# Kernel optimization log

Hardware: AMD Instinct MI355X
Metric: run time of the kernel (lower is better)

## Reference

```python
import jax, jax.numpy as jnp
import numpy as np

N_GROUP, D, DFF = 8, 256, 1024
T = 131072  # total routed tokens


def setup_inputs() -> dict:
    key = jax.random.key(0)
    k_x, k_g, k_u, k_d = jax.random.split(key, 4)
    # kaiming_uniform_(a=sqrt(5)) over fan_in == second-to-last dim
    def kaiming(k, shape, fan_in):
        bound = 1.0 / np.sqrt(fan_in)
        return jax.random.uniform(k, shape, jnp.float32, -bound, bound)
    x = jax.random.normal(k_x, (T, D), jnp.float32)
    weight_gate = kaiming(k_g, (N_GROUP, D, DFF), D)
    weight_up = kaiming(k_u, (N_GROUP, D, DFF), D)
    weight_down = kaiming(k_d, (N_GROUP, DFF, D), DFF)
    # cumulative group end offsets; uniform groups of T // N_GROUP tokens
    offs = (jnp.arange(1, N_GROUP + 1, dtype=jnp.int32) * (T // N_GROUP))
    return {"x": x, "weight_gate": weight_gate, "weight_up": weight_up,
            "weight_down": weight_down, "offs": offs}


def reference(x, weight_gate, weight_up, weight_down, offs):
    # Grouped GLU: for tokens in group g, y = silu(x @ Wg_gate) * (x @ Wg_up) @ Wg_down.
    # offs encodes uniform group boundaries (offs[i] = (i+1)*T/G), so the grouped
    # GEMM is a batched matmul over the expert axis after a reshape.
    G = weight_gate.shape[0]
    t, d = x.shape
    xg = x.reshape(G, t // G, d)                                  # [G, Tg, d]
    z_gate = jnp.einsum('gtd,gdf->gtf', xg, weight_gate)          # [G, Tg, dff]
    z_up = jnp.einsum('gtd,gdf->gtf', xg, weight_up)
    h = jax.nn.silu(z_gate) * z_up
    y = jnp.einsum('gtf,gfd->gtd', h, weight_down)                # [G, Tg, d]
    return y.reshape(t, d)
```

## Files before the change

### kernel.cpp

```cpp
#include <hip/hip_runtime.h>

typedef __bf16 bf16x8 __attribute__((ext_vector_type(8)));
typedef float f32x16 __attribute__((ext_vector_type(16)));
typedef unsigned int u32x4 __attribute__((ext_vector_type(4)));

#define NGROUP 8
#define DMODEL 256
#define DFF    1024
#define TTOT   131072
#define TGRP   (TTOT / NGROUP)
#define MTILE  256
#define NCHUNK 32

__device__ __forceinline__ unsigned int f2bf(float f) {
    unsigned int x = __builtin_bit_cast(unsigned int, f);
    return (x + 0x7fffu + ((x >> 16) & 1u)) >> 16;
}
__device__ __forceinline__ unsigned int pack2(float lo, float hi) {
    return f2bf(lo) | (f2bf(hi) << 16);
}
__device__ __forceinline__ unsigned int cvtpk(float lo, float hi) {
    unsigned int r;
    asm("v_cvt_pk_bf16_f32 %0, %1, %2" : "=v"(r) : "v"(lo), "v"(hi));
    return r;
}

__device__ __forceinline__ void g2l(const void* g, void* l) {
    __builtin_amdgcn_global_load_lds(
        (const __attribute__((address_space(1))) unsigned int*)g,
        (__attribute__((address_space(3))) unsigned int*)l, 16, 0, 0);
}

__global__ void k_prep_w(const float* __restrict__ wg, const float* __restrict__ wu,
                         const float* __restrict__ wd, u32x4* __restrict__ out) {
    int t = blockIdx.x * 256 + threadIdx.x;
    int lane = t & 63;
    int q = lane >> 5, l31 = lane & 31;
    int fg = t >> 6;
    int fid = fg % 48;
    int gc  = fg / 48;
    int c = gc & 31, g = gc >> 5;
    u32x4 v;
    if (fid < 32) {
        const float* w = (fid < 16) ? wg : wu;
        int ks = fid & 15;
        const float* src = w + (size_t)(g * 256 + ks * 16 + q * 8) * 1024 + c * 32 + l31;
        v = u32x4{ pack2(src[0],        src[1024]),
                   pack2(src[2 * 1024], src[3 * 1024]),
                   pack2(src[4 * 1024], src[5 * 1024]),
                   pack2(src[6 * 1024], src[7 * 1024]) };
    } else {
        int idx = fid - 32;
        int ks2 = idx >> 3, nb = idx & 7;
        const float* src = wd + (size_t)(g * 1024 + c * 32 + ks2 * 16 + q * 4) * 256 + nb * 32 + l31;
        v = u32x4{ pack2(src[0 * 256],  src[1 * 256]),
                   pack2(src[2 * 256],  src[3 * 256]),
                   pack2(src[8 * 256],  src[9 * 256]),
                   pack2(src[10 * 256], src[11 * 256]) };
    }
    out[t] = v;
}

#define MFMA(A, B, C) __builtin_amdgcn_mfma_f32_32x32x16_bf16( \
        __builtin_bit_cast(bf16x8, A), __builtin_bit_cast(bf16x8, B), C, 0, 0, 0)

__global__ __launch_bounds__(512, 2)
void k_glu(const float* __restrict__ x,
           const u32x4* __restrict__ wcomb,
           float* __restrict__ y) {
    __shared__ u32x4 smem[9216];

    const int tid  = threadIdx.x;
    const int lane = tid & 63;
    const int w    = tid >> 6;
    const int q    = lane >> 5;
    const int l31  = lane & 31;

    const int g    = blockIdx.x & 7;
    const int m0   = g * TGRP + (blockIdx.x >> 3) * MTILE;
    const int tok  = m0 + w * 32 + l31;

    const u32x4* wcg = wcomb + (size_t)(g * 32) * 3072;

    #pragma unroll
    for (int i = 0; i < 6; ++i) {
        int off = i * 512 + w * 64;
        g2l(wcg + off + lane, smem + off);
    }
    #pragma unroll
    for (int i = 0; i < 6; ++i) {
        int off = i * 512 + w * 64;
        g2l(wcg + 3072 + off + lane, smem + 3072 + off);
    }
    u32x4 xf[16];
    {
        const float* xrow = x + (size_t)tok * DMODEL + q * 8;
        #pragma unroll
        for (int ks = 0; ks < 16; ++ks) {
            float4 a = *(const float4*)(xrow + ks * 16);
            float4 b = *(const float4*)(xrow + ks * 16 + 4);
            xf[ks] = u32x4{ cvtpk(a.x, a.y), cvtpk(a.z, a.w),
                            cvtpk(b.x, b.y), cvtpk(b.z, b.w) };
        }
    }

    f32x16 acc[8];
    #pragma unroll
    for (int nb = 0; nb < 8; ++nb)
        #pragma unroll
        for (int i = 0; i < 16; ++i) acc[nb][i] = 0.0f;

    asm volatile("s_waitcnt vmcnt(0)" ::: "memory");
    __builtin_amdgcn_s_barrier();
    asm volatile("" ::: "memory");

    u32x4 A0, A1;

    {
        const u32x4* sb = smem;
        f32x16 zg, zu;
        #pragma unroll
        for (int i = 0; i < 16; ++i) { zg[i] = 0.0f; zu[i] = 0.0f; }
        #pragma unroll
        for (int ks = 0; ks < 16; ++ks) {
            const u32x4 a1 = sb[ks * 64 + lane];
            const u32x4 a2 = sb[1024 + ks * 64 + lane];
            zg = MFMA(a1, xf[ks], zg);
            zu = MFMA(a2, xf[ks], zu);
        }
        float hv[16];
        #pragma unroll
        for (int i = 0; i < 16; ++i) {
            const float gv = zg[i];
            const float s  = __builtin_amdgcn_rcpf(1.0f + __expf(-gv));
            hv[i] = gv * s * zu[i];
        }
        A0 = u32x4{ cvtpk(hv[0], hv[1]),   cvtpk(hv[2], hv[3]),
                    cvtpk(hv[4], hv[5]),   cvtpk(hv[6], hv[7]) };
        A1 = u32x4{ cvtpk(hv[8], hv[9]),   cvtpk(hv[10], hv[11]),
                    cvtpk(hv[12], hv[13]), cvtpk(hv[14], hv[15]) };
    }

    int bc = 1, bp = 0, bn = 2;
    for (int c = 1; c < NCHUNK; ++c) {
        const u32x4* sbc = smem + bc * 3072;
        const u32x4* sbp = smem + bp * 3072;

        asm volatile("s_waitcnt vmcnt(0)" ::: "memory");
        __builtin_amdgcn_s_barrier();
        asm volatile("" ::: "memory");

        if (c + 1 < NCHUNK) {
            u32x4* db = smem + bn * 3072;
            const u32x4* gsrc = wcg + (size_t)(c + 1) * 3072;
            #pragma unroll
            for (int i = 0; i < 6; ++i) {
                int off = i * 512 + w * 64;
                g2l(gsrc + off + lane, db + off);
            }
        }

        f32x16 zg, zu;
        #pragma unroll
        for (int i = 0; i < 16; ++i) { zg[i] = 0.0f; zu[i] = 0.0f; }
        #pragma unroll
        for (int ks = 0; ks < 16; ++ks) {
            const u32x4 a1 = sbc[ks * 64 + lane];
            const u32x4 a2 = sbc[1024 + ks * 64 + lane];
            const u32x4 bd = sbp[2048 + ks * 64 + lane];
            zg = MFMA(a1, xf[ks], zg);
            zu = MFMA(a2, xf[ks], zu);
            if (ks < 8) acc[ks]     = MFMA(A0, bd, acc[ks]);
            else        acc[ks - 8] = MFMA(A1, bd, acc[ks - 8]);
        }

        float hv[16];
        #pragma unroll
        for (int i = 0; i < 16; ++i) {
            const float gv = zg[i];
            const float s  = __builtin_amdgcn_rcpf(1.0f + __expf(-gv));
            hv[i] = gv * s * zu[i];
        }
        A0 = u32x4{ cvtpk(hv[0], hv[1]),   cvtpk(hv[2], hv[3]),
                    cvtpk(hv[4], hv[5]),   cvtpk(hv[6], hv[7]) };
        A1 = u32x4{ cvtpk(hv[8], hv[9]),   cvtpk(hv[10], hv[11]),
                    cvtpk(hv[12], hv[13]), cvtpk(hv[14], hv[15]) };

        const int t = bp; bp = bc; bc = bn; bn = t;
    }

    {
        const u32x4* sbp = smem + bp * 3072;
        #pragma unroll
        for (int ks = 0; ks < 16; ++ks) {
            const u32x4 bd = sbp[2048 + ks * 64 + lane];
            if (ks < 8) acc[ks]     = MFMA(A0, bd, acc[ks]);
            else        acc[ks - 8] = MFMA(A1, bd, acc[ks - 8]);
        }
    }

    float* yp = y + (size_t)(m0 + w * 32) * DMODEL;
    #pragma unroll
    for (int nb = 0; nb < 8; ++nb) {
        const int col = nb * 32 + l31;
        #pragma unroll
        for (int r = 0; r < 16; ++r) {
            const int row = (r & 3) + (r >> 2) * 8 + q * 4;
            yp[(size_t)row * DMODEL + col] = acc[nb][r];
        }
    }
}

extern "C" void kernel_launch(void* const* d_in, const int* in_sizes, int n_in,
                              void* d_out, int out_size, void* d_ws, size_t ws_size,
                              hipStream_t stream) {
    const float* x  = (const float*)d_in[0];
    const float* wg = (const float*)d_in[1];
    const float* wu = (const float*)d_in[2];
    const float* wd = (const float*)d_in[3];
    float* y = (float*)d_out;

    u32x4* wcomb = (u32x4*)d_ws;

    k_prep_w<<<dim3(3072), dim3(256), 0, stream>>>(wg, wu, wd, wcomb);
    k_glu<<<dim3(512), dim3(512), 0, stream>>>(x, wcomb, y);
}
```

Measured before the change: 414.9 us.

## Give each wave two 32-token row tiles and prefetch weight chunks two ahead

Blocks shrink from 512 to 256 threads and each wave now processes 64 tokens as two 32-row tiles. Every weight fragment read from LDS therefore feeds two MFMAs, halving LDS traffic per FLOP. The cross-chunk software pipeline, which overlapped the down-projection of chunk c-1 with the gate/up of chunk c, is replaced by a triple buffer that prefetches two chunks ahead with partial vmcnt waits. s_setprio is added around the MFMA blocks. The cost is much higher register use: two x fragment sets and two accumulator sets per wave, with launch bounds set to one block. Occupancy also drops to 4 waves per block.

```diff
diff --git a/kernel.cpp b/kernel.cpp
--- a/kernel.cpp
+++ b/kernel.cpp
@@ -64,7 +64,7 @@
 #define MFMA(A, B, C) __builtin_amdgcn_mfma_f32_32x32x16_bf16( \
         __builtin_bit_cast(bf16x8, A), __builtin_bit_cast(bf16x8, B), C, 0, 0, 0)
 
-__global__ __launch_bounds__(512, 2)
+__global__ __launch_bounds__(256, 1)
 void k_glu(const float* __restrict__ x,
            const u32x4* __restrict__ wcomb,
            float* __restrict__ y) {
@@ -78,135 +78,151 @@
 
     const int g    = blockIdx.x & 7;
     const int m0   = g * TGRP + (blockIdx.x >> 3) * MTILE;
-    const int tok  = m0 + w * 32 + l31;
+    const int tok0 = m0 + w * 64 + l31;
+    const int tok1 = tok0 + 32;
 
     const u32x4* wcg = wcomb + (size_t)(g * 32) * 3072;
 
     #pragma unroll
-    for (int i = 0; i < 6; ++i) {
-        int off = i * 512 + w * 64;
+    for (int i = 0; i < 12; ++i) {
+        int off = i * 256 + w * 64;
         g2l(wcg + off + lane, smem + off);
     }
     #pragma unroll
-    for (int i = 0; i < 6; ++i) {
-        int off = i * 512 + w * 64;
+    for (int i = 0; i < 12; ++i) {
+        int off = i * 256 + w * 64;
         g2l(wcg + 3072 + off + lane, smem + 3072 + off);
     }
-    u32x4 xf[16];
+    u32x4 xf0[16], xf1[16];
     {
-        const float* xrow = x + (size_t)tok * DMODEL + q * 8;
+        const float* xr0 = x + (size_t)tok0 * DMODEL + q * 8;
+        const float* xr1 = x + (size_t)tok1 * DMODEL + q * 8;
         #pragma unroll
         for (int ks = 0; ks < 16; ++ks) {
-            float4 a = *(const float4*)(xrow + ks * 16);
-            float4 b = *(const float4*)(xrow + ks * 16 + 4);
-            xf[ks] = u32x4{ cvtpk(a.x, a.y), cvtpk(a.z, a.w),
-                            cvtpk(b.x, b.y), cvtpk(b.z, b.w) };
-        }
-    }
-
-    f32x16 acc[8];
+            float4 a = *(const float4*)(xr0 + ks * 16);
+            float4 b = *(const float4*)(xr0 + ks * 16 + 4);
+            xf0[ks] = u32x4{ cvtpk(a.x, a.y), cvtpk(a.z, a.w),
+                             cvtpk(b.x, b.y), cvtpk(b.z, b.w) };
+            float4 cfour = *(const float4*)(xr1 + ks * 16);
+            float4 d = *(const float4*)(xr1 + ks * 16 + 4);
+            xf1[ks] = u32x4{ cvtpk(cfour.x, cfour.y), cvtpk(cfour.z, cfour.w),
+                             cvtpk(d.x, d.y), cvtpk(d.z, d.w) };
+        }
+    }
+
+    f32x16 acc0[8], acc1[8];
     #pragma unroll
     for (int nb = 0; nb < 8; ++nb)
         #pragma unroll
-        for (int i = 0; i < 16; ++i) acc[nb][i] = 0.0f;
+        for (int i = 0; i < 16; ++i) { acc0[nb][i] = 0.0f; acc1[nb][i] = 0.0f; }
 
     asm volatile("s_waitcnt vmcnt(0)" ::: "memory");
     __builtin_amdgcn_s_barrier();
     asm volatile("" ::: "memory");
 
-    u32x4 A0, A1;
-
-    {
-        const u32x4* sb = smem;
-        f32x16 zg, zu;
-        #pragma unroll
-        for (int i = 0; i < 16; ++i) { zg[i] = 0.0f; zu[i] = 0.0f; }
-        #pragma unroll
-        for (int ks = 0; ks < 16; ++ks) {
-            const u32x4 a1 = sb[ks * 64 + lane];
-            const u32x4 a2 = sb[1024 + ks * 64 + lane];
-            zg = MFMA(a1, xf[ks], zg);
-            zu = MFMA(a2, xf[ks], zu);
-        }
-        float hv[16];
-        #pragma unroll
-        for (int i = 0; i < 16; ++i) {
-            const float gv = zg[i];
-            const float s  = __builtin_amdgcn_rcpf(1.0f + __expf(-gv));
-            hv[i] = gv * s * zu[i];
-        }
-        A0 = u32x4{ cvtpk(hv[0], hv[1]),   cvtpk(hv[2], hv[3]),
-                    cvtpk(hv[4], hv[5]),   cvtpk(hv[6], hv[7]) };
-        A1 = u32x4{ cvtpk(hv[8], hv[9]),   cvtpk(hv[10], hv[11]),
-                    cvtpk(hv[12], hv[13]), cvtpk(hv[14], hv[15]) };
-    }
-
-    int bc = 1, bp = 0, bn = 2;
-    for (int c = 1; c < NCHUNK; ++c) {
+    int bc = 0;
+    for (int c = 0; c < NCHUNK; ++c) {
         const u32x4* sbc = smem + bc * 3072;
-        const u32x4* sbp = smem + bp * 3072;
-
-        asm volatile("s_waitcnt vmcnt(0)" ::: "memory");
-        __builtin_amdgcn_s_barrier();
-        asm volatile("" ::: "memory");
-
-        if (c + 1 < NCHUNK) {
+
+        if (c > 0) {
+            if (c <= NCHUNK - 2) {
+                asm volatile("s_waitcnt vmcnt(12)" ::: "memory");
+            } else {
+                asm volatile("s_waitcnt vmcnt(0)" ::: "memory");
+            }
+            __builtin_amdgcn_s_barrier();
+            asm volatile("" ::: "memory");
+        }
+
+        if (c + 2 < NCHUNK) {
+            const int bn = (bc + 2 >= 3) ? bc - 1 : bc + 2;
             u32x4* db = smem + bn * 3072;
-            const u32x4* gsrc = wcg + (size_t)(c + 1) * 3072;
-            #pragma unroll
-            for (int i = 0; i < 6; ++i) {
-                int off = i * 512 + w * 64;
+            const u32x4* gsrc = wcg + (size_t)(c + 2) * 3072;
+            #pragma unroll
+            for (int i = 0; i < 12; ++i) {
+                int off = i * 256 + w * 64;
                 g2l(gsrc + off + lane, db + off);
             }
         }
 
-        f32x16 zg, zu;
-        #pragma unroll
-        for (int i = 0; i < 16; ++i) { zg[i] = 0.0f; zu[i] = 0.0f; }
+        f32x16 zg0, zu0, zg1, zu1;
+        #pragma unroll
+        for (int i = 0; i < 16; ++i) { zg0[i] = 0.0f; zu0[i] = 0.0f; zg1[i] = 0.0f; zu1[i] = 0.0f; }
+        __builtin_amdgcn_s_setprio(1);
         #pragma unroll
         for (int ks = 0; ks < 16; ++ks) {
             const u32x4 a1 = sbc[ks * 64 + lane];
             const u32x4 a2 = sbc[1024 + ks * 64 + lane];
-            const u32x4 bd = sbp[2048 + ks * 64 + lane];
-            zg = MFMA(a1, xf[ks], zg);
-            zu = MFMA(a2, xf[ks], zu);
-            if (ks < 8) acc[ks]     = MFMA(A0, bd, acc[ks]);
-            else        acc[ks - 8] = MFMA(A1, bd, acc[ks - 8]);
-        }
-
-        float hv[16];
-        #pragma unroll
-        for (int i = 0; i < 16; ++i) {
-            const float gv = zg[i];
-            const float s  = __builtin_amdgcn_rcpf(1.0f + __expf(-gv));
-            hv[i] = gv * s * zu[i];
-        }
-        A0 = u32x4{ cvtpk(hv[0], hv[1]),   cvtpk(hv[2], hv[3]),
-                    cvtpk(hv[4], hv[5]),   cvtpk(hv[6], hv[7]) };
-        A1 = u32x4{ cvtpk(hv[8], hv[9]),   cvtpk(hv[10], hv[11]),
-                    cvtpk(hv[12], hv[13]), cvtpk(hv[14], hv[15]) };
-
-        const int t = bp; bp = bc; bc = bn; bn = t;
+            zg0 = MFMA(a1, xf0[ks], zg0);
+            zg1 = MFMA(a1, xf1[ks], zg1);
+            zu0 = MFMA(a2, xf0[ks], zu0);
+            zu1 = MFMA(a2, xf1[ks], zu1);
+        }
+        __builtin_amdgcn_s_setprio(0);
+
+        u32x4 A00, A01, A10, A11;
+        {
+            float hv[16];
+            #pragma unroll
+            for (int i = 0; i < 16; ++i) {
+                const float gv = zg0[i];
+                const float s  = __builtin_amdgcn_rcpf(1.0f + __expf(-gv));
+                hv[i] = gv * s * zu0[i];
+            }
+            A00 = u32x4{ cvtpk(hv[0], hv[1]),   cvtpk(hv[2], hv[3]),
+                         cvtpk(hv[4], hv[5]),   cvtpk(hv[6], hv[7]) };
+            A01 = u32x4{ cvtpk(hv[8], hv[9]),   cvtpk(hv[10], hv[11]),
+                         cvtpk(hv[12], hv[13]), cvtpk(hv[14], hv[15]) };
+            #pragma unroll
+            for (int i = 0; i < 16; ++i) {
+                const float gv = zg1[i];
+                const float s  = __builtin_amdgcn_rcpf(1.0f + __expf(-gv));
+                hv[i] = gv * s * zu1[i];
+            }
+            A10 = u32x4{ cvtpk(hv[0], hv[1]),   cvtpk(hv[2], hv[3]),
+                         cvtpk(hv[4], hv[5]),   cvtpk(hv[6], hv[7]) };
+            A11 = u32x4{ cvtpk(hv[8], hv[9]),   cvtpk(hv[10], hv[11]),
+                         cvtpk(hv[12], hv[13]), cvtpk(hv[14], hv[15]) };
+        }
+
+        __builtin_amdgcn_s_setprio(1);
+        #pragma unroll
+        for (int fi = 0; fi < 8; ++fi) {
+            const u32x4 bd = sbc[2048 + fi * 64 + lane];
+            acc0[fi] = MFMA(A00, bd, acc0[fi]);
+            acc1[fi] = MFMA(A10, bd, acc1[fi]);
+        }
+        #pragma unroll
+        for (int fi = 0; fi < 8; ++fi) {
+            const u32x4 bd = sbc[2048 + (8 + fi) * 64 + lane];
+            acc0[fi] = MFMA(A01, bd, acc0[fi]);
+            acc1[fi] = MFMA(A11, bd, acc1[fi]);
+        }
+        __builtin_amdgcn_s_setprio(0);
+
+        bc = (bc == 2) ? 0 : bc + 1;
     }
 
     {
-        const u32x4* sbp = smem + bp * 3072;
-        #pragma unroll
-        for (int ks = 0; ks < 16; ++ks) {
-            const u32x4 bd = sbp[2048 + ks * 64 + lane];
-            if (ks < 8) acc[ks]     = MFMA(A0, bd, acc[ks]);
-            else        acc[ks - 8] = MFMA(A1, bd, acc[ks - 8]);
-        }
-    }
-
-    float* yp = y + (size_t)(m0 + w * 32) * DMODEL;
-    #pragma unroll
-    for (int nb = 0; nb < 8; ++nb) {
-        const int col = nb * 32 + l31;
-        #pragma unroll
-        for (int r = 0; r < 16; ++r) {
-            const int row = (r & 3) + (r >> 2) * 8 + q * 4;
-            yp[(size_t)row * DMODEL + col] = acc[nb][r];
+        float* yp = y + (size_t)(m0 + w * 64) * DMODEL;
+        #pragma unroll
+        for (int nb = 0; nb < 8; ++nb) {
+            const int col = nb * 32 + l31;
+            #pragma unroll
+            for (int r = 0; r < 16; ++r) {
+                const int row = (r & 3) + (r >> 2) * 8 + q * 4;
+                yp[(size_t)row * DMODEL + col] = acc0[nb][r];
+            }
+        }
+        float* yq = yp + 32 * DMODEL;
+        #pragma unroll
+        for (int nb = 0; nb < 8; ++nb) {
+            const int col = nb * 32 + l31;
+            #pragma unroll
+            for (int r = 0; r < 16; ++r) {
+                const int row = (r & 3) + (r >> 2) * 8 + q * 4;
+                yq[(size_t)row * DMODEL + col] = acc1[nb][r];
+            }
         }
     }
 }
@@ -223,5 +239,5 @@
     u32x4* wcomb = (u32x4*)d_ws;
 
     k_prep_w<<<dim3(3072), dim3(256), 0, stream>>>(wg, wu, wd, wcomb);
-    k_glu<<<dim3(512), dim3(512), 0, stream>>>(x, wcomb, y);
-}
+    k_glu<<<dim3(512), dim3(256), 0, stream>>>(x, wcomb, y);
+}
```

After: 546.0 us. 31.6% more time.

## Split fused GLU into two GEMM kernels with bf16 intermediate buffer

Applied to the files above, without the earlier changes.

Replaces the single fused GLU kernel with two kernels. The first computes gate/up projections and SiLU for 64 tokens per wave and writes h in MFMA-fragment layout to a workspace buffer. The second runs the down projection with a 2x4 wave tiling and a triple-buffered, two-chunk-ahead load pipeline. This targets the low MFMA reuse of the fused kernel, where each wave handled 32 tokens, at the cost of writing and re-reading a 256 MB bf16 intermediate. The old fused kernel remains as a fallback when the workspace is too small.

```diff
diff --git a/kernel.cpp b/kernel.cpp
--- a/kernel.cpp
+++ b/kernel.cpp
@@ -9,8 +9,8 @@
 #define DFF    1024
 #define TTOT   131072
 #define TGRP   (TTOT / NGROUP)
-#define MTILE  256
 #define NCHUNK 32
+
 
 __device__ __forceinline__ unsigned int f2bf(float f) {
     unsigned int x = __builtin_bit_cast(unsigned int, f);
@@ -30,6 +30,9 @@
         (const __attribute__((address_space(1))) unsigned int*)g,
         (__attribute__((address_space(3))) unsigned int*)l, 16, 0, 0);
 }
+
+#define MFMA(A, B, C) __builtin_amdgcn_mfma_f32_32x32x16_bf16( \
+        __builtin_bit_cast(bf16x8, A), __builtin_bit_cast(bf16x8, B), C, 0, 0, 0)
 
 __global__ void k_prep_w(const float* __restrict__ wg, const float* __restrict__ wu,
                          const float* __restrict__ wd, u32x4* __restrict__ out) {
@@ -61,14 +64,10 @@
     out[t] = v;
 }
 
-#define MFMA(A, B, C) __builtin_amdgcn_mfma_f32_32x32x16_bf16( \
-        __builtin_bit_cast(bf16x8, A), __builtin_bit_cast(bf16x8, B), C, 0, 0, 0)
-
 __global__ __launch_bounds__(512, 2)
-void k_glu(const float* __restrict__ x,
-           const u32x4* __restrict__ wcomb,
-           float* __restrict__ y) {
-    __shared__ u32x4 smem[9216];
+void k_gemm1(const float* __restrict__ x, const u32x4* __restrict__ wcomb,
+             u32x4* __restrict__ hout) {
+    __shared__ u32x4 smem[4096];
 
     const int tid  = threadIdx.x;
     const int lane = tid & 63;
@@ -77,21 +76,213 @@
     const int l31  = lane & 31;
 
     const int g    = blockIdx.x & 7;
-    const int m0   = g * TGRP + (blockIdx.x >> 3) * MTILE;
-    const int tok  = m0 + w * 32 + l31;
+    const int m0   = g * TGRP + (blockIdx.x >> 3) * 512;
+    const int tok0 = m0 + w * 64 + l31;
+    const int tok1 = tok0 + 32;
+    const size_t tb0 = (size_t)((m0 >> 5) + w * 2);
 
     const u32x4* wcg = wcomb + (size_t)(g * 32) * 3072;
 
     #pragma unroll
-    for (int i = 0; i < 6; ++i) {
+    for (int i = 0; i < 4; ++i) {
         int off = i * 512 + w * 64;
         g2l(wcg + off + lane, smem + off);
     }
-    #pragma unroll
-    for (int i = 0; i < 6; ++i) {
-        int off = i * 512 + w * 64;
-        g2l(wcg + 3072 + off + lane, smem + 3072 + off);
-    }
+
+    u32x4 xf0[16], xf1[16];
+    {
+        const float* xr0 = x + (size_t)tok0 * DMODEL + q * 8;
+        const float* xr1 = x + (size_t)tok1 * DMODEL + q * 8;
+        #pragma unroll
+        for (int ks = 0; ks < 16; ++ks) {
+            float4 a = *(const float4*)(xr0 + ks * 16);
+            float4 b = *(const float4*)(xr0 + ks * 16 + 4);
+            xf0[ks] = u32x4{ cvtpk(a.x, a.y), cvtpk(a.z, a.w),
+                             cvtpk(b.x, b.y), cvtpk(b.z, b.w) };
+            float4 e = *(const float4*)(xr1 + ks * 16);
+            float4 d = *(const float4*)(xr1 + ks * 16 + 4);
+            xf1[ks] = u32x4{ cvtpk(e.x, e.y), cvtpk(e.z, e.w),
+                             cvtpk(d.x, d.y), cvtpk(d.z, d.w) };
+        }
+    }
+
+    for (int c = 0; c < NCHUNK; ++c) {
+        const u32x4* sbc = smem + (c & 1) * 2048;
+
+        asm volatile("s_waitcnt vmcnt(0)" ::: "memory");
+        __builtin_amdgcn_s_barrier();
+        asm volatile("" ::: "memory");
+
+        if (c + 1 < NCHUNK) {
+            u32x4* db = smem + ((c + 1) & 1) * 2048;
+            const u32x4* gsrc = wcg + (size_t)(c + 1) * 3072;
+            #pragma unroll
+            for (int i = 0; i < 4; ++i) {
+                int off = i * 512 + w * 64;
+                g2l(gsrc + off + lane, db + off);
+            }
+        }
+
+        f32x16 zg0, zu0, zg1, zu1;
+        #pragma unroll
+        for (int i = 0; i < 16; ++i) { zg0[i] = 0.0f; zu0[i] = 0.0f; zg1[i] = 0.0f; zu1[i] = 0.0f; }
+        __builtin_amdgcn_s_setprio(1);
+        #pragma unroll
+        for (int ks = 0; ks < 16; ++ks) {
+            const u32x4 a1 = sbc[ks * 64 + lane];
+            const u32x4 a2 = sbc[1024 + ks * 64 + lane];
+            zg0 = MFMA(a1, xf0[ks], zg0);
+            zg1 = MFMA(a1, xf1[ks], zg1);
+            zu0 = MFMA(a2, xf0[ks], zu0);
+            zu1 = MFMA(a2, xf1[ks], zu1);
+        }
+        __builtin_amdgcn_s_setprio(0);
+
+        u32x4 A00, A01, A10, A11;
+        {
+            float hv[16];
+            #pragma unroll
+            for (int i = 0; i < 16; ++i) {
+                const float gv = zg0[i];
+                const float s  = __builtin_amdgcn_rcpf(1.0f + __expf(-gv));
+                hv[i] = gv * s * zu0[i];
+            }
+            A00 = u32x4{ cvtpk(hv[0], hv[1]),   cvtpk(hv[2], hv[3]),
+                         cvtpk(hv[4], hv[5]),   cvtpk(hv[6], hv[7]) };
+            A01 = u32x4{ cvtpk(hv[8], hv[9]),   cvtpk(hv[10], hv[11]),
+                         cvtpk(hv[12], hv[13]), cvtpk(hv[14], hv[15]) };
+            #pragma unroll
+            for (int i = 0; i < 16; ++i) {
+                const float gv = zg1[i];
+                const float s  = __builtin_amdgcn_rcpf(1.0f + __expf(-gv));
+                hv[i] = gv * s * zu1[i];
+            }
+            A10 = u32x4{ cvtpk(hv[0], hv[1]),   cvtpk(hv[2], hv[3]),
+                         cvtpk(hv[4], hv[5]),   cvtpk(hv[6], hv[7]) };
+            A11 = u32x4{ cvtpk(hv[8], hv[9]),   cvtpk(hv[10], hv[11]),
+                         cvtpk(hv[12], hv[13]), cvtpk(hv[14], hv[15]) };
+        }
+
+        u32x4* hp = hout + (tb0 * 64 + 2 * c) * 64 + lane;
+        hp[0]    = A00;
+        hp[64]   = A01;
+        hp[4096] = A10;
+        hp[4160] = A11;
+    }
+}
+
+__global__ __launch_bounds__(512, 2)
+void k_gemm2(const u32x4* __restrict__ hbuf, const u32x4* __restrict__ wcomb,
+             float* __restrict__ y) {
+    __shared__ u32x4 smem[6144];
+
+    const int tid  = threadIdx.x;
+    const int lane = tid & 63;
+    const int w    = tid >> 6;
+    const int q    = lane >> 5;
+    const int l31  = lane & 31;
+    const int wr   = w >> 2;
+    const int wc   = w & 3;
+
+    const int g  = blockIdx.x & 7;
+    const int mb = blockIdx.x >> 3;
+    const int m0 = g * TGRP + mb * 256;
+    const int TB0 = m0 >> 5;
+
+    const u32x4* wcg = wcomb + (size_t)(g * 32) * 3072;
+
+    auto stage = [&](int c, u32x4* buf) {
+        #pragma unroll
+        for (int i = 0; i < 4; ++i) {
+            const int j = w * 4 + i;
+            const u32x4* src = (j < 16)
+                ? hbuf + ((size_t)(TB0 + (j >> 1)) * 64 + 2 * c + (j & 1)) * 64
+                : wcg + (size_t)c * 3072 + 2048 + (size_t)(j - 16) * 64;
+            g2l(src + lane, buf + j * 64);
+        }
+    };
+
+    stage(0, smem);
+    stage(1, smem + 2048);
+
+    f32x16 acc[8];
+    #pragma unroll
+    for (int t = 0; t < 8; ++t)
+        #pragma unroll
+        for (int i = 0; i < 16; ++i) acc[t][i] = 0.0f;
+
+    int bc = 0;
+    for (int c = 0; c < NCHUNK; ++c) {
+        const u32x4* sb = smem + bc * 2048;
+
+        if (c < NCHUNK - 1) {
+            asm volatile("s_waitcnt vmcnt(4)" ::: "memory");
+        } else {
+            asm volatile("s_waitcnt vmcnt(0)" ::: "memory");
+        }
+        __builtin_amdgcn_s_barrier();
+        asm volatile("" ::: "memory");
+
+        if (c + 2 < NCHUNK) {
+            const int bn = (bc + 2 >= 3) ? bc - 1 : bc + 2;
+            stage(c + 2, smem + bn * 2048);
+        }
+
+        __builtin_amdgcn_s_setprio(1);
+        #pragma unroll
+        for (int ks2 = 0; ks2 < 2; ++ks2) {
+            const u32x4 ha0 = sb[((wr * 4 + 0) * 2 + ks2) * 64 + lane];
+            const u32x4 ha1 = sb[((wr * 4 + 1) * 2 + ks2) * 64 + lane];
+            const u32x4 ha2 = sb[((wr * 4 + 2) * 2 + ks2) * 64 + lane];
+            const u32x4 ha3 = sb[((wr * 4 + 3) * 2 + ks2) * 64 + lane];
+            const u32x4 bd0 = sb[1024 + (ks2 * 8 + wc * 2 + 0) * 64 + lane];
+            const u32x4 bd1 = sb[1024 + (ks2 * 8 + wc * 2 + 1) * 64 + lane];
+            acc[0] = MFMA(ha0, bd0, acc[0]);
+            acc[1] = MFMA(ha0, bd1, acc[1]);
+            acc[2] = MFMA(ha1, bd0, acc[2]);
+            acc[3] = MFMA(ha1, bd1, acc[3]);
+            acc[4] = MFMA(ha2, bd0, acc[4]);
+            acc[5] = MFMA(ha2, bd1, acc[5]);
+            acc[6] = MFMA(ha3, bd0, acc[6]);
+            acc[7] = MFMA(ha3, bd1, acc[7]);
+        }
+        __builtin_amdgcn_s_setprio(0);
+
+        bc = (bc == 2) ? 0 : bc + 1;
+    }
+
+    #pragma unroll
+    for (int tb = 0; tb < 4; ++tb) {
+        #pragma unroll
+        for (int db = 0; db < 2; ++db) {
+            float* yp = y + (size_t)(m0 + wr * 128 + tb * 32) * DMODEL + wc * 64 + db * 32;
+            const f32x16 a = acc[tb * 2 + db];
+            #pragma unroll
+            for (int r = 0; r < 16; ++r) {
+                const int row = (r & 3) + (r >> 2) * 8 + q * 4;
+                yp[(size_t)row * DMODEL + l31] = a[r];
+            }
+        }
+    }
+}
+
+__global__ __launch_bounds__(512, 2)
+void k_glu(const float* __restrict__ x, const u32x4* __restrict__ wcomb,
+           float* __restrict__ y) {
+    __shared__ u32x4 smem[9216];
+    const int tid  = threadIdx.x;
+    const int lane = tid & 63;
+    const int w    = tid >> 6;
+    const int q    = lane >> 5;
+    const int l31  = lane & 31;
+    const int g    = blockIdx.x & 7;
+    const int m0   = g * TGRP + (blockIdx.x >> 3) * 256;
+    const int tok  = m0 + w * 32 + l31;
+    const u32x4* wcg = wcomb + (size_t)(g * 32) * 3072;
+    #pragma unroll
+    for (int i = 0; i < 6; ++i) { int off = i * 512 + w * 64; g2l(wcg + off + lane, smem + off); }
+    #pragma unroll
+    for (int i = 0; i < 6; ++i) { int off = i * 512 + w * 64; g2l(wcg + 3072 + off + lane, smem + 3072 + off); }
     u32x4 xf[16];
     {
         const float* xrow = x + (size_t)tok * DMODEL + q * 8;
@@ -99,23 +290,18 @@
         for (int ks = 0; ks < 16; ++ks) {
             float4 a = *(const float4*)(xrow + ks * 16);
             float4 b = *(const float4*)(xrow + ks * 16 + 4);
-            xf[ks] = u32x4{ cvtpk(a.x, a.y), cvtpk(a.z, a.w),
-                            cvtpk(b.x, b.y), cvtpk(b.z, b.w) };
-        }
-    }
-
+            xf[ks] = u32x4{ cvtpk(a.x, a.y), cvtpk(a.z, a.w), cvtpk(b.x, b.y), cvtpk(b.z, b.w) };
+        }
+    }
     f32x16 acc[8];
     #pragma unroll
     for (int nb = 0; nb < 8; ++nb)
         #pragma unroll
         for (int i = 0; i < 16; ++i) acc[nb][i] = 0.0f;
-
     asm volatile("s_waitcnt vmcnt(0)" ::: "memory");
     __builtin_amdgcn_s_barrier();
     asm volatile("" ::: "memory");
-
     u32x4 A0, A1;
-
     {
         const u32x4* sb = smem;
         f32x16 zg, zu;
@@ -135,31 +321,22 @@
             const float s  = __builtin_amdgcn_rcpf(1.0f + __expf(-gv));
             hv[i] = gv * s * zu[i];
         }
-        A0 = u32x4{ cvtpk(hv[0], hv[1]),   cvtpk(hv[2], hv[3]),
-                    cvtpk(hv[4], hv[5]),   cvtpk(hv[6], hv[7]) };
-        A1 = u32x4{ cvtpk(hv[8], hv[9]),   cvtpk(hv[10], hv[11]),
-                    cvtpk(hv[12], hv[13]), cvtpk(hv[14], hv[15]) };
-    }
-
+        A0 = u32x4{ cvtpk(hv[0], hv[1]), cvtpk(hv[2], hv[3]), cvtpk(hv[4], hv[5]), cvtpk(hv[6], hv[7]) };
+        A1 = u32x4{ cvtpk(hv[8], hv[9]), cvtpk(hv[10], hv[11]), cvtpk(hv[12], hv[13]), cvtpk(hv[14], hv[15]) };
+    }
     int bc = 1, bp = 0, bn = 2;
     for (int c = 1; c < NCHUNK; ++c) {
         const u32x4* sbc = smem + bc * 3072;
         const u32x4* sbp = smem + bp * 3072;
-
         asm volatile("s_waitcnt vmcnt(0)" ::: "memory");
         __builtin_amdgcn_s_barrier();
         asm volatile("" ::: "memory");
-
         if (c + 1 < NCHUNK) {
             u32x4* db = smem + bn * 3072;
             const u32x4* gsrc = wcg + (size_t)(c + 1) * 3072;
             #pragma unroll
-            for (int i = 0; i < 6; ++i) {
-                int off = i * 512 + w * 64;
-                g2l(gsrc + off + lane, db + off);
-            }
-        }
-
+            for (int i = 0; i < 6; ++i) { int off = i * 512 + w * 64; g2l(gsrc + off + lane, db + off); }
+        }
         f32x16 zg, zu;
         #pragma unroll
         for (int i = 0; i < 16; ++i) { zg[i] = 0.0f; zu[i] = 0.0f; }
@@ -173,7 +350,6 @@
             if (ks < 8) acc[ks]     = MFMA(A0, bd, acc[ks]);
             else        acc[ks - 8] = MFMA(A1, bd, acc[ks - 8]);
         }
-
         float hv[16];
         #pragma unroll
         for (int i = 0; i < 16; ++i) {
@@ -181,14 +357,10 @@
             const float s  = __builtin_amdgcn_rcpf(1.0f + __expf(-gv));
             hv[i] = gv * s * zu[i];
         }
-        A0 = u32x4{ cvtpk(hv[0], hv[1]),   cvtpk(hv[2], hv[3]),
-                    cvtpk(hv[4], hv[5]),   cvtpk(hv[6], hv[7]) };
-        A1 = u32x4{ cvtpk(hv[8], hv[9]),   cvtpk(hv[10], hv[11]),
-                    cvtpk(hv[12], hv[13]), cvtpk(hv[14], hv[15]) };
-
+        A0 = u32x4{ cvtpk(hv[0], hv[1]), cvtpk(hv[2], hv[3]), cvtpk(hv[4], hv[5]), cvtpk(hv[6], hv[7]) };
+        A1 = u32x4{ cvtpk(hv[8], hv[9]), cvtpk(hv[10], hv[11]), cvtpk(hv[12], hv[13]), cvtpk(hv[14], hv[15]) };
         const int t = bp; bp = bc; bc = bn; bn = t;
     }
-
     {
         const u32x4* sbp = smem + bp * 3072;
         #pragma unroll
@@ -198,7 +370,6 @@
             else        acc[ks - 8] = MFMA(A1, bd, acc[ks - 8]);
         }
     }
-
     float* yp = y + (size_t)(m0 + w * 32) * DMODEL;
     #pragma unroll
     for (int nb = 0; nb < 8; ++nb) {
@@ -221,7 +392,15 @@
     float* y = (float*)d_out;
 
     u32x4* wcomb = (u32x4*)d_ws;
+    u32x4* hbuf  = wcomb + 786432;
+
+    const size_t need = (size_t)786432 * 16 + (size_t)4096 * 64 * 64 * 16;
 
     k_prep_w<<<dim3(3072), dim3(256), 0, stream>>>(wg, wu, wd, wcomb);
-    k_glu<<<dim3(512), dim3(512), 0, stream>>>(x, wcomb, y);
-}
+    if (ws_size >= need) {
+        k_gemm1<<<dim3(256), dim3(512), 0, stream>>>(x, wcomb, hbuf);
+        k_gemm2<<<dim3(512), dim3(512), 0, stream>>>(hbuf, wcomb, y);
+    } else {
+        k_glu<<<dim3(512), dim3(512), 0, stream>>>(x, wcomb, y);
+    }
+}
```

Result: slower. 567.5 us (+36.8%).
